# Kernel optimization log

Measured on AMD Instinct MI355X. Metric: run time of the kernel, lower is better.

Reference implementation:

```python
import jax, jax.numpy as jnp
import numpy as np

B, T, N, D = 32, 12, 325, 64
H = 4           # geo_num_heads == t_num_heads
HD = D // H     # head_dim = 16
M_SP = 32       # spatial frequency modes (min(32, N//2))
M_T = T // 2    # temporal frequency modes (all low modes)
SCALE = HD ** -0.5


def _lin(x, W):
    # torch nn.Linear (no bias): y = x @ W.T, W: [out, in]
    return jnp.einsum('btnd,ed->btne', x, W)


def _spatial(x, Wq, Wk, Wv, weights_Q, sp_modes):
    # FEDformer-style frequency attention over the node axis N
    q, k, v = _lin(x, Wq), _lin(x, Wk), _lin(x, Wv)          # [B,T,N,D]
    prep = lambda y: y.reshape(B, T, N, H, HD).transpose(0, 1, 3, 4, 2)  # [B,T,H,HD,N]
    qn = prep(q) / jnp.linalg.norm(q)   # global Frobenius norm (torch.norm with no dim)
    kn = prep(k) / jnp.linalg.norm(k)
    vn = prep(v)
    # rfft over nodes, gather selected modes (scatter-into-zeros in torch == gather here
    # since target indices are 0..M-1)
    qf = jnp.fft.rfft(qn, axis=-1)[..., sp_modes]            # [B,T,H,HD,M] c64
    kf = jnp.fft.rfft(kn, axis=-1)[..., sp_modes]
    vf = jnp.fft.rfft(vn, axis=-1)[..., sp_modes]
    M = M_SP
    qg = qf.transpose(0, 1, 2, 4, 3)[:, :, :, :, None, :]    # [B,T,H,M,1,HD]
    wq = jnp.broadcast_to(weights_Q.astype(jnp.complex64), (B, T, H, M, M - 1, HD))
    q_cat = jnp.concatenate([qg, wq], axis=4)                # [B,T,H,M,M,HD]
    kg = kf.transpose(0, 1, 2, 4, 3)[:, :, :, None, :, :]    # [B,T,H,1,M,HD]
    att = kg * jnp.conj(q_cat) * SCALE                       # [B,T,H,M,M,HD] c64
    att = jax.nn.softmax(jnp.abs(att), axis=-2).astype(jnp.complex64)
    att = att.transpose(0, 1, 2, 3, 5, 4)                    # [B,T,H,M,HD,M]
    vg = vf[:, :, :, None, :, :]                             # [B,T,H,1,HD,M]
    out = (vg * jnp.conj(att)).mean(axis=3)                  # [B,T,H,HD,M]
    out_ft = jnp.zeros((B, T, H, HD, N // 2 + 1), jnp.complex64).at[..., sp_modes].set(out)
    y = jnp.fft.irfft(out_ft, n=N, axis=-1)                  # [B,T,H,HD,N]
    return y.transpose(0, 1, 4, 2, 3).reshape(B, T, N, D)


def _temporal(x, Wq, Wk, Wv, weights_Q_t, t_modes):
    # frequency attention over the time axis T with causal (tril) mask.
    # NOTE: torch reshapes the [B,T,N,D] buffer directly as [B,N,T,H,HD] (raw view),
    # so we replicate that exact buffer reinterpretation.
    q, k, v = _lin(x, Wq), _lin(x, Wk), _lin(x, Wv)
    prep = lambda y: y.reshape(B, N, T, H, HD).transpose(0, 1, 3, 4, 2)  # [B,N,H,HD,T]
    qn = prep(q); kn = prep(k); vn = prep(v)
    qn = qn / jnp.linalg.norm(qn)
    kn = kn / jnp.linalg.norm(kn)
    qf = jnp.fft.rfft(qn, axis=-1)[..., t_modes]             # [B,N,H,HD,Mt]
    kf = jnp.fft.rfft(kn, axis=-1)[..., t_modes]
    vf = jnp.fft.rfft(vn, axis=-1)[..., t_modes]
    Mt = M_T
    qg = qf.transpose(0, 1, 2, 4, 3)[:, :, :, :, None, :]    # [B,N,H,Mt,1,HD]
    wq = jnp.broadcast_to(weights_Q_t.astype(jnp.complex64), (B, N, H, Mt, Mt - 1, HD))
    q_cat = jnp.concatenate([qg, wq], axis=4)                # [B,N,H,Mt,Mt,HD]
    kg = kf.transpose(0, 1, 2, 4, 3)[:, :, :, :, None, :]    # [B,N,H,Mt,1,HD] (unsqueeze(4) in torch)
    att = kg * jnp.conj(q_cat) * SCALE                       # [B,N,H,Mt,Mt,HD]
    att = att.transpose(0, 1, 2, 5, 3, 4)                    # [B,N,H,HD,Mt,Mt]
    mask = jnp.tril(jnp.ones((Mt, Mt), jnp.float32))
    att = att * mask                                         # zero above diagonal
    attw = jax.nn.softmax(jnp.abs(att), axis=-1).astype(jnp.complex64)
    vg = vf[..., None]                                       # [B,N,H,HD,Mt,1]
    out = (vg * jnp.conj(attw)).mean(axis=-1)                # [B,N,H,HD,Mt]
    out_ft = jnp.zeros((B, N, H, HD, T // 2 + 1), jnp.complex64).at[..., t_modes].set(out)
    y = jnp.fft.irfft(out_ft, n=T, axis=-1)                  # [B,N,H,HD,T]
    return y.transpose(0, 4, 1, 2, 3).reshape(B, T, N, D)


def _gcn(x, adj, W_fc1, W_mlp, b_mlp):
    a = adj / jnp.sum(adj, axis=1, keepdims=True)            # row-normalized
    agg = jnp.einsum('btkd,nk->btnd', x, a)
    h = jnp.einsum('btnd,ed->btne', agg, W_fc1)              # fc1 (no bias)
    return jnp.einsum('btnd,ed->btne', h, W_mlp) + b_mlp     # mlp (bias)


def _forward(x, adj, Wq_geo, Wk_geo, Wv_geo, Wq_t, Wk_t, Wv_t,
             W_fc1, W_mlp, b_mlp, weights_Q, weights_Q_t, sp_modes, t_modes):
    gcn_out = _gcn(x, adj, W_fc1, W_mlp, b_mlp)
    sp_x = _spatial(x, Wq_geo, Wk_geo, Wv_geo, weights_Q, sp_modes)
    te_x = _temporal(x, Wq_t, Wk_t, Wv_t, weights_Q_t, t_modes)
    return gcn_out + sp_x + te_x   # proj_drop is identity (p=0)


def setup_inputs() -> dict:
    key = jax.random.key(0)
    ks = jax.random.split(key, 13)
    w = lambda k, s: jax.random.normal(k, s, dtype=jnp.float32) * 0.05
    rng = np.random.default_rng(0)
    sp_modes = np.sort(rng.permutation(N // 2)[:M_SP]).astype(np.int32)
    t_modes = np.arange(M_T, dtype=np.int32)  # modes_T == T//2 selects all low modes
    return {
        'x': jax.random.normal(ks[0], (B, T, N, D), dtype=jnp.float32),
        'adj': jax.random.uniform(ks[1], (N, N), dtype=jnp.float32),
        'Wq_geo': w(ks[2], (D, D)), 'Wk_geo': w(ks[3], (D, D)), 'Wv_geo': w(ks[4], (D, D)),
        'Wq_t': w(ks[5], (D, D)), 'Wk_t': w(ks[6], (D, D)), 'Wv_t': w(ks[7], (D, D)),
        'W_fc1': w(ks[8], (D, D)), 'W_mlp': w(ks[9], (D, D)), 'b_mlp': w(ks[10], (D,)),
        'weights_Q': jax.random.normal(ks[11], (M_SP, M_SP - 1, HD), dtype=jnp.float32),
        'weights_Q_t': jax.random.normal(ks[12], (M_T, M_T - 1, HD), dtype=jnp.float32),
        'sp_modes': jnp.asarray(sp_modes),
        't_modes': jnp.asarray(t_modes),
    }


def reference(x, adj, Wq_geo, Wk_geo, Wv_geo, Wq_t, Wk_t, Wv_t,
              W_fc1, W_mlp, b_mlp, weights_Q, weights_Q_t, sp_modes, t_modes):
    return _forward(x, adj, Wq_geo, Wk_geo, Wv_geo, Wq_t, Wk_t, Wv_t,
                    W_fc1, W_mlp, b_mlp, weights_Q, weights_Q_t, sp_modes, t_modes)
```

## Files before the change

kernel.cpp:

```cpp
#include <hip/hip_runtime.h>


typedef unsigned short u16;
typedef short short8 __attribute__((ext_vector_type(8)));
typedef float floatx4 __attribute__((ext_vector_type(4)));

__device__ __forceinline__ u16 f2bf(float f) {
  union { float fp; unsigned int u; } v; v.fp = f;
  unsigned int x = v.u;
  x += 0x7FFF + ((x >> 16) & 1);
  return (u16)(x >> 16);
}

constexpr size_t OFF_NORM = 4096;
constexpr size_t OFF_WQA  = 8208;
constexpr size_t OFF_ANB  = 24080;
constexpr size_t OFF_TB   = 81280;
constexpr size_t OFF_T2   = 102080;
constexpr size_t OFF_OFT  = 112480;
constexpr size_t OFF_XCT  = 898912;
constexpr size_t OFF_WBB  = 5224288;
constexpr size_t OFF_WSPB = 5226336;
constexpr size_t OFF_WVTB = 5232480;
constexpr size_t OFF_XA   = 13211488;

__global__ __launch_bounds__(256) void k_prep(const float* __restrict__ x,
                                              const float* __restrict__ Wmlp,
                                              const float* __restrict__ Wfc1,
                                              const float* __restrict__ wQ,
                                              const float* __restrict__ Wq,
                                              const float* __restrict__ Wk,
                                              const float* __restrict__ Wv,
                                              const int* __restrict__ sp_modes,
                                              float* __restrict__ ws) {
  __shared__ float red[256];
  __shared__ __align__(16) u16 XA[128 * 72];
  const int tid = threadIdx.x;
  const int blk = blockIdx.x;
  u16* WBBu = (u16*)(ws + OFF_WBB);
  if (blk >= 22) {
    const int blk2 = blk - 22;
    const int wv = tid >> 6, lane = tid & 63, lc = lane & 15, quad = lane >> 4;
    const size_t base = (size_t)blk2 * 128;
    for (int i = tid; i < 2048; i += 256) {
      const int row = i >> 4, e0 = (i & 15) * 4;
      const float4 v = *(const float4*)(x + (base + row) * 64 + e0);
      u16* dst = &XA[row * 72 + e0];
      dst[0] = f2bf(v.x); dst[1] = f2bf(v.y); dst[2] = f2bf(v.z); dst[3] = f2bf(v.w);
    }
    __syncthreads();
    floatx4 acc[2][8] = {};
#pragma unroll
    for (int kc = 0; kc < 2; ++kc) {
      short8 af[2];
#pragma unroll
      for (int mi = 0; mi < 2; ++mi)
        af[mi] = *(const short8*)&XA[(32 * wv + 16 * mi + lc) * 72 + kc * 32 + quad * 8];
#pragma unroll
      for (int ni = 0; ni < 8; ++ni) {
        const int g = (ni & 3) * 16 + lc;
        const float* src = ((ni < 4) ? Wq : Wk) + (size_t)g * 64 + kc * 32 + quad * 8;
        float v8[8];
        *(float4*)v8 = *(const float4*)src;
        *(float4*)(v8 + 4) = *(const float4*)(src + 4);
        short8 bf_;
#pragma unroll
        for (int u = 0; u < 8; ++u) bf_[u] = (short)f2bf(v8[u]);
#pragma unroll
        for (int mi = 0; mi < 2; ++mi)
          acc[mi][ni] = __builtin_amdgcn_mfma_f32_16x16x32_bf16(af[mi], bf_, acc[mi][ni], 0, 0, 0);
      }
    }
    float sq = 0.f, sk = 0.f;
#pragma unroll
    for (int mi = 0; mi < 2; ++mi)
#pragma unroll
      for (int reg = 0; reg < 4; ++reg) {
#pragma unroll
        for (int ni = 0; ni < 4; ++ni) {
          const float v = acc[mi][ni][reg];
          sq = fmaf(v, v, sq);
        }
#pragma unroll
        for (int ni = 4; ni < 8; ++ni) {
          const float v = acc[mi][ni][reg];
          sk = fmaf(v, v, sk);
        }
      }
    for (int off = 32; off > 0; off >>= 1) {
      sq += __shfl_down(sq, off);
      sk += __shfl_down(sk, off);
    }
    if (lane == 0) { red[wv] = sq; red[8 + wv] = sk; }
    __syncthreads();
    if (tid == 0) {
      atomicAdd(&ws[OFF_NORM + 0], red[0] + red[1] + red[2] + red[3]);
      atomicAdd(&ws[OFF_NORM + 1], red[8] + red[9] + red[10] + red[11]);
    }
    return;
  }
  if (blk == 0) {
    for (int o = tid; o < 4096; o += 256) {
      int g = o >> 6, dd = o & 63;
      float s = 0.f;
      for (int e = 0; e < 64; ++e)
        s = fmaf(Wmlp[g * 64 + e], Wfc1[e * 64 + dd], s);
      WBBu[o] = f2bf(s);
    }
  } else if (blk < 9) {
    for (int i = (blk - 1) * 256 + tid; i < 15872; i += 2048)
      ws[OFF_WQA + i] = fabsf(wQ[i]);
  } else if (blk < 21) {
    const int j = blk - 9;
    u16* T2B = (u16*)(ws + OFF_T2);
    u16* TB = (u16*)(ws + OFF_TB);
    for (int jj = j; jj < 32; jj += 12) {
      const int f = sp_modes[jj];
      const float wgt = (f == 0) ? 1.f : 2.f;
      const int row_re = 8 * (jj >> 2) + (jj & 3);
      const int row_im = row_re + 4;
      for (int n = tid; n < 352; n += 256) {
        float c = 0.f, s = 0.f;
        if (n < 325) {
          int mm = (f * n) % 325;
          float th = 6.283185307179586f * (float)mm * (1.f / 325.f);
          c = cosf(th);
          s = sinf(th);
        }
        TB[(size_t)row_re * 352 + n] = f2bf(c);
        TB[(size_t)row_im * 352 + n] = f2bf(-s);
        if (n < 325) {
          T2B[(size_t)n * 64 + 2 * jj] = f2bf(wgt * (1.f / 325.f) * c);
          T2B[(size_t)n * 64 + 2 * jj + 1] = f2bf(-wgt * (1.f / 325.f) * s);
        }
      }
    }
  } else {
    u16* WSPBu = (u16*)(ws + OFF_WSPB);
    for (int i = tid; i < 12288; i += 256) {
      const int r = i >> 6, e = i & 63;
      const float* src = (r < 64) ? Wq : (r < 128) ? Wk : Wv;
      WSPBu[i] = f2bf(src[(size_t)(r & 63) * 64 + e]);
    }
  }
}

__global__ __launch_bounds__(256) void k_mega(const float* __restrict__ x,
                                              const float* __restrict__ adj,
                                              const float* __restrict__ Wvt,
                                              float* __restrict__ ws) {
  __shared__ __align__(16) float smem[12800];
  const int tid = threadIdx.x;
  const int blk = blockIdx.x;
  const int lane = tid & 63, wv = tid >> 6;
  const int lc = lane & 15, quad = lane >> 4;

  if (blk < 384) {
    const int bt = blk;
    u16* XBu = (u16*)smem;
    const float g_nq = ws[OFF_NORM + 0];
    const float g_nk = ws[OFF_NORM + 1];

    const u16* TB = (const u16*)(ws + OFF_TB);
    const u16* WSPBu = (const u16*)(ws + OFF_WSPB);
    const float* xb = x + (size_t)bt * 20800;
    const int br = tid & 31, be0 = (tid >> 5) * 8;

    {
      float va[4][8];
#pragma unroll
      for (int g = 0; g < 3; ++g) {
        const int nkc = (g < 2) ? 4 : 3;
#pragma unroll
        for (int u = 0; u < 4; ++u) {
          if (u >= nkc) break;
          const int k0 = (g * 4 + u) * 32;
          if (k0 + br < 325) {
            const float* src = xb + (size_t)(k0 + br) * 64 + be0;
            *(float4*)&va[u][0] = *(const float4*)src;
            *(float4*)&va[u][4] = *(const float4*)(src + 4);
          } else {
#pragma unroll
            for (int w = 0; w < 8; ++w) va[u][w] = 0.f;
          }
        }
#pragma unroll
        for (int u = 0; u < 4; ++u) {
          if (u >= nkc) break;
          const int k0 = (g * 4 + u) * 32;
#pragma unroll
          for (int w = 0; w < 8; ++w)
            XBu[(be0 + w) * 360 + k0 + br] = f2bf(va[u][w]);
        }
      }
    }
    __syncthreads();

    floatx4 accA[4] = {};
#pragma unroll
    for (int kc = 0; kc < 11; ++kc) {
      const short8 af = *(const short8*)&TB[(size_t)(16 * wv + lc) * 352 + kc * 32 + quad * 8];
#pragma unroll
      for (int t = 0; t < 4; ++t) {
        const short8 bf_ = *(const short8*)&XBu[(t * 16 + lc) * 360 + kc * 32 + quad * 8];
        accA[t] = __builtin_amdgcn_mfma_f32_16x16x32_bf16(af, bf_, accA[t], 0, 0, 0);
      }
    }
    __syncthreads();

    u16* xfl2 = XBu;
#pragma unroll
    for (int t = 0; t < 4; ++t)
#pragma unroll
      for (int r = 0; r < 4; ++r)
        xfl2[(t >> 1) * 2560 + (16 * wv + quad * 4 + r) * 40 + (t & 1) * 16 + lc] =
            f2bf(accA[t][r]);
    __syncthreads();

    floatx4 acc2[12] = {};
#pragma unroll
    for (int kc2 = 0; kc2 < 2; ++kc2) {
      const short8 af2 = *(const short8*)&xfl2[kc2 * 2560 + (16 * wv + lc) * 40 + quad * 8];
#pragma unroll
      for (int t = 0; t < 12; ++t) {
        const short8 bf2 = *(const short8*)&WSPBu[(t * 16 + lc) * 64 + kc2 * 32 + quad * 8];
        acc2[t] = __builtin_amdgcn_mfma_f32_16x16x32_bf16(af2, bf2, acc2[t], 0, 0, 0);
      }
    }
    __syncthreads();

    float* sq_q = smem + 2560;
    float* sq_k = smem + 4608;
    float* vfre = smem + 6656;
    float* vfim = smem + 8704;
    float* wbar = smem + 10752;
    for (int i = tid; i < 2048; i += 256) wbar[i] = 0.f;
    {
      const int fb = 8 * wv + ((quad >= 2) ? 4 : 0);
      const int isim = quad & 1;
#pragma unroll
      for (int t = 0; t < 12; ++t) {
        const int mat = t >> 2;
        const int d = (t & 3) * 16 + lc;
#pragma unroll
        for (int r = 0; r < 4; ++r) {
          const float v = acc2[t][r];
          if (mat == 2) {
            if (isim) vfim[(fb + r) * 64 + d] = v;
            else vfre[(fb + r) * 64 + d] = v;
          } else {
            const float s2 = v * v + __shfl_xor(v * v, 16);
            if (!isim) {
              if (mat == 0) sq_q[(fb + r) * 64 + d] = s2;
              else sq_k[(fb + r) * 64 + d] = s2;
            }
          }
        }
      }
    }
    __syncthreads();
    const float inv_nq = rsqrtf(g_nq);
    const float inv_nk = rsqrtf(g_nk);
    for (int i = tid; i < 2048; i += 256)
      sq_k[i] = 0.25f * inv_nk * sqrtf(sq_k[i]);
    __syncthreads();
    {
      const int d = tid & 63, fb2 = tid >> 6, hd = d & 15;
      const float* wqa = ws + OFF_WQA;
      float wacc[32];
#pragma unroll
      for (int j = 0; j < 32; ++j) wacc[j] = 0.f;
      for (int r8 = 0; r8 < 8; ++r8) {
        const int m = fb2 + (r8 << 2);
        const float aq = inv_nq * sqrtf(sq_q[m * 64 + d]);
        float sv[32];
        float mx = -1e30f;
#pragma unroll
        for (int j = 0; j < 32; ++j) {
          const float a = (j == 0) ? aq : wqa[(m * 31 + (j - 1)) * 16 + hd];
          const float s = sq_k[j * 64 + d] * a;
          sv[j] = s;
          mx = fmaxf(mx, s);
        }
        float sum = 0.f;
#pragma unroll
        for (int j = 0; j < 32; ++j) {
          const float ev = __expf(sv[j] - mx);
          sv[j] = ev;
          sum += ev;
        }
        const float sc = 0.03125f / sum;
#pragma unroll
        for (int j = 0; j < 32; ++j) wacc[j] += sv[j] * sc;
      }
#pragma unroll
      for (int j = 0; j < 32; ++j) atomicAdd(&wbar[j * 64 + d], wacc[j]);
    }
    __syncthreads();
    unsigned int* OFTu = (unsigned int*)(ws + OFF_OFT) + (size_t)bt * 2048;
    for (int i2 = tid; i2 < 2048; i2 += 256) {
      const int d = i2 >> 5, j = i2 & 31;
      const float w = wbar[j * 64 + d];
      const unsigned int lo = f2bf(vfre[j * 64 + d] * w);
      const unsigned int hi = f2bf(vfim[j * 64 + d] * w);
      OFTu[i2] = lo | (hi << 16);
    }
  } else if (blk < 1359) {
    const int blk2 = blk - 384;
    u16* XAu = (u16*)smem;
    const size_t base = (size_t)blk2 * 128;
    const u16* WBBu = (const u16*)(ws + OFF_WBB);

    for (int i = tid; i < 2048; i += 256) {
      const int row = i >> 4, e0 = (i & 15) * 4;
      const float4 v = *(const float4*)(x + (base + row) * 64 + e0);
      u16* dst = &XAu[row * 72 + e0];
      dst[0] = f2bf(v.x); dst[1] = f2bf(v.y); dst[2] = f2bf(v.z); dst[3] = f2bf(v.w);
    }
    __syncthreads();

    floatx4 acc[2][4] = {};
#pragma unroll
    for (int kc = 0; kc < 2; ++kc) {
      short8 af[2];
#pragma unroll
      for (int mi = 0; mi < 2; ++mi)
        af[mi] = *(const short8*)&XAu[(32 * wv + 16 * mi + lc) * 72 + kc * 32 + quad * 8];
#pragma unroll
      for (int ni = 0; ni < 4; ++ni) {
        const short8 bf_ = *(const short8*)&WBBu[(ni * 16 + lc) * 64 + kc * 32 + quad * 8];
#pragma unroll
        for (int mi = 0; mi < 2; ++mi)
          acc[mi][ni] = __builtin_amdgcn_mfma_f32_16x16x32_bf16(af[mi], bf_, acc[mi][ni], 0, 0, 0);
      }
    }
    __syncthreads();

    u16* xcT = XAu;
#pragma unroll
    for (int ni = 0; ni < 4; ++ni)
#pragma unroll
      for (int mi = 0; mi < 2; ++mi)
#pragma unroll
        for (int reg = 0; reg < 4; ++reg)
          xcT[(ni * 16 + lc) * 132 + 32 * wv + 16 * mi + quad * 4 + reg] =
              f2bf(acc[mi][ni][reg]);
    __syncthreads();
    u16* XCT = (u16*)(ws + OFF_XCT);
    for (int i = tid; i < 8192; i += 256) {
      const int d = i >> 7, r = i & 127;
      const unsigned int row = (unsigned int)(base + r);
      const unsigned int bt = row / 325u;
      const unsigned int n = row - bt * 325u;
      XCT[(size_t)bt * 22528 + (size_t)d * 352 + n] = xcT[d * 132 + r];
    }
  } else if (blk < 2009) {
    const int idx = (blk - 1359) * 256 + tid;
    if (idx >= 32 * 325 * 16) return;
    const int dq = idx & 15;
    const int n = (idx >> 4) % 325;
    const int b = idx / (16 * 325);
    const float* xp = x + ((size_t)b * 3900 + (size_t)n * 12) * 64 + dq * 4;
    float4 s = make_float4(0.f, 0.f, 0.f, 0.f);
    float sign = 1.f;
    for (int k = 0; k < 12; ++k) {
      const float4 v = *(const float4*)(xp + (size_t)k * 64);
      s.x += sign * v.x; s.y += sign * v.y; s.z += sign * v.z; s.w += sign * v.w;
      sign = -sign;
    }
    *(float4*)(ws + OFF_XA + ((size_t)b * 325 + n) * 64 + dq * 4) = s;
  } else if (blk < 2334) {
    const int n = blk - 2009;
    float* red = smem;
    float p = 0.f;
    for (int k = tid; k < 325; k += 256) p += adj[n * 325 + k];
    red[tid] = p;
    __syncthreads();
    for (int s2 = 128; s2 > 0; s2 >>= 1) {
      if (tid < s2) red[tid] += red[tid + s2];
      __syncthreads();
    }
    const float inv = 1.f / red[0];
    u16* ANB = (u16*)(ws + OFF_ANB);
    for (int k = tid; k < 352; k += 256)
      ANB[(size_t)n * 352 + k] = (k < 325) ? f2bf(adj[n * 325 + k] * inv) : (u16)0;
  } else if (blk < 2430) {
    const int idx = (blk - 2334) * 256 + tid;
    u16* p = (u16*)(ws + OFF_XCT) + (size_t)(idx >> 6) * 22528 + (size_t)(idx & 63) * 352;
    for (int c = 325; c < 352; ++c) p[c] = 0;
  } else {
    u16* WVTBu = (u16*)(ws + OFF_WVTB);
    for (int i = tid; i < 4096; i += 256) WVTBu[i] = f2bf(Wvt[i]);
  }
}

__global__ __launch_bounds__(256) void k_final2(const float* __restrict__ x,
                                                const float* __restrict__ bmlp,
                                                float* __restrict__ ws,
                                                float* __restrict__ out) {
  const int tid = threadIdx.x;
  const int bt = blockIdx.x / 3, mc = blockIdx.x % 3;
  const int m0 = mc * 128;
  const int wave = tid >> 6, lane = tid & 63;
  const int quad = lane >> 4, lc = lane & 15;

  const u16* ANB = (const u16*)(ws + OFF_ANB);
  const u16* T2B = (const u16*)(ws + OFF_T2);
  const u16* XCT = (const u16*)(ws + OFF_XCT) + (size_t)bt * 22528;
  const u16* OFT = (const u16*)(ws + OFF_OFT) + (size_t)bt * 4096;
  const u16* WVTBu = (const u16*)(ws + OFF_WVTB);

  const int b = bt / 12, t = bt - b * 12;
  const float sgn12 = ((t & 1) ? -1.f : 1.f) * (1.f / 12.f);

  floatx4 acc[2][4] = {};

#pragma unroll
  for (int c13 = 0; c13 < 13; ++c13) {
    const bool gcn = (c13 < 11);
    const u16* Asrc = gcn ? ANB : T2B;
    const int astr = gcn ? 352 : 64;
    const int acol = gcn ? c13 * 32 : (c13 - 11) * 32;
    const u16* Bsrc = gcn ? XCT : OFT;
    const int bstr = gcn ? 352 : 64;
    short8 af[2], bf_[4];
#pragma unroll
    for (int mi = 0; mi < 2; ++mi) {
      const int gr = m0 + wave * 32 + mi * 16 + lc;
      short8 a = {};
      if (gr < 325)
        a = *(const short8*)&Asrc[(size_t)gr * astr + acol + quad * 8];
      af[mi] = a;
    }
#pragma unroll
    for (int ni = 0; ni < 4; ++ni)
      bf_[ni] = *(const short8*)&Bsrc[(size_t)(ni * 16 + lc) * bstr + acol + quad * 8];
#pragma unroll
    for (int mi = 0; mi < 2; ++mi)
#pragma unroll
      for (int ni = 0; ni < 4; ++ni)
        acc[mi][ni] = __builtin_amdgcn_mfma_f32_16x16x32_bf16(
            af[mi], bf_[ni], acc[mi][ni], 0, 0, 0);
  }

#pragma unroll
  for (int kc = 0; kc < 2; ++kc) {
    const int k0 = kc * 32 + quad * 8;
    short8 af[2];
#pragma unroll
    for (int mi = 0; mi < 2; ++mi) {
      const int nr = m0 + wave * 32 + mi * 16 + lc;
      short8 a = {};
      if (nr < 325) {
        const float* xp = x + ((size_t)b * 3900 + (size_t)nr * 12 + t) * 64 + k0;
        const float* xap = ws + OFF_XA + ((size_t)b * 325 + nr) * 64 + k0;
        float xv[8], av[8];
        *(float4*)xv = *(const float4*)xp;
        *(float4*)(xv + 4) = *(const float4*)(xp + 4);
        *(float4*)av = *(const float4*)xap;
        *(float4*)(av + 4) = *(const float4*)(xap + 4);
#pragma unroll
        for (int u = 0; u < 8; ++u)
          a[u] = (short)f2bf((xv[u] - sgn12 * av[u]) * (1.f / 6.f));
      }
      af[mi] = a;
    }
#pragma unroll
    for (int ni = 0; ni < 4; ++ni) {
      const short8 bf_ = *(const short8*)&WVTBu[(size_t)(ni * 16 + lc) * 64 + k0];
#pragma unroll
      for (int mi = 0; mi < 2; ++mi)
        acc[mi][ni] = __builtin_amdgcn_mfma_f32_16x16x32_bf16(
            af[mi], bf_, acc[mi][ni], 0, 0, 0);
    }
  }

#pragma unroll
  for (int ni = 0; ni < 4; ++ni) {
    const int d = ni * 16 + lc;
    const float bias = bmlp[d];
#pragma unroll
    for (int mi = 0; mi < 2; ++mi) {
#pragma unroll
      for (int reg = 0; reg < 4; ++reg) {
        const int n = m0 + wave * 32 + mi * 16 + quad * 4 + reg;
        if (n >= 325) continue;
        out[((size_t)bt * 325 + n) * 64 + d] = acc[mi][ni][reg] + bias;
      }
    }
  }
}

extern "C" void kernel_launch(void* const* d_in, const int* in_sizes, int n_in,
                              void* d_out, int out_size, void* d_ws, size_t ws_size,
                              hipStream_t stream) {
  const float* x = (const float*)d_in[0];
  const float* adj = (const float*)d_in[1];
  const float* Wq_g = (const float*)d_in[2];
  const float* Wk_g = (const float*)d_in[3];
  const float* Wv_g = (const float*)d_in[4];
  const float* Wv_t = (const float*)d_in[7];
  const float* Wfc1 = (const float*)d_in[8];
  const float* Wmlp = (const float*)d_in[9];
  const float* bmlp = (const float*)d_in[10];
  const float* wQ = (const float*)d_in[11];
  const int* sp_modes = (const int*)d_in[13];
  float* ws = (float*)d_ws;
  float* out = (float*)d_out;

  (void)in_sizes; (void)n_in; (void)out_size; (void)ws_size;

  hipMemsetAsync(ws + OFF_NORM, 0, 2 * sizeof(float), stream);
  k_prep<<<997, 256, 0, stream>>>(x, Wmlp, Wfc1, wQ, Wq_g, Wk_g, Wv_g,
                                  sp_modes, ws);
  k_mega<<<2431, 256, 0, stream>>>(x, adj, Wv_t, ws);
  k_final2<<<1152, 256, 0, stream>>>(x, bmlp, ws, out);
}
```

Measured before the change: 250.9 us.

## Fuse norm reduction into mega kernel and move spectral softmax into final kernel

```diff
diff --git a/kernel.cpp b/kernel.cpp
--- a/kernel.cpp
+++ b/kernel.cpp
@@ -17,15 +17,17 @@
 constexpr size_t OFF_ANB  = 24080;
 constexpr size_t OFF_TB   = 81280;
 constexpr size_t OFF_T2   = 102080;
-constexpr size_t OFF_OFT  = 112480;
 constexpr size_t OFF_XCT  = 898912;
 constexpr size_t OFF_WBB  = 5224288;
-constexpr size_t OFF_WSPB = 5226336;
-constexpr size_t OFF_WVTB = 5232480;
+constexpr size_t OFF_WSPB = 5230432;
+constexpr size_t OFF_WVTB = 5236576;
+constexpr size_t OFF_SQQ  = 5240000;
+constexpr size_t OFF_SQK  = 6026432;
+constexpr size_t OFF_VFR  = 6812864;
+constexpr size_t OFF_VFI  = 7599296;
 constexpr size_t OFF_XA   = 13211488;
 
-__global__ __launch_bounds__(256) void k_prep(const float* __restrict__ x,
-                                              const float* __restrict__ Wmlp,
+__global__ __launch_bounds__(256) void k_prep(const float* __restrict__ Wmlp,
                                               const float* __restrict__ Wfc1,
                                               const float* __restrict__ wQ,
                                               const float* __restrict__ Wq,
@@ -33,73 +35,11 @@
                                               const float* __restrict__ Wv,
                                               const int* __restrict__ sp_modes,
                                               float* __restrict__ ws) {
-  __shared__ float red[256];
-  __shared__ __align__(16) u16 XA[128 * 72];
   const int tid = threadIdx.x;
   const int blk = blockIdx.x;
   u16* WBBu = (u16*)(ws + OFF_WBB);
-  if (blk >= 22) {
-    const int blk2 = blk - 22;
-    const int wv = tid >> 6, lane = tid & 63, lc = lane & 15, quad = lane >> 4;
-    const size_t base = (size_t)blk2 * 128;
-    for (int i = tid; i < 2048; i += 256) {
-      const int row = i >> 4, e0 = (i & 15) * 4;
-      const float4 v = *(const float4*)(x + (base + row) * 64 + e0);
-      u16* dst = &XA[row * 72 + e0];
-      dst[0] = f2bf(v.x); dst[1] = f2bf(v.y); dst[2] = f2bf(v.z); dst[3] = f2bf(v.w);
-    }
-    __syncthreads();
-    floatx4 acc[2][8] = {};
-#pragma unroll
-    for (int kc = 0; kc < 2; ++kc) {
-      short8 af[2];
-#pragma unroll
-      for (int mi = 0; mi < 2; ++mi)
-        af[mi] = *(const short8*)&XA[(32 * wv + 16 * mi + lc) * 72 + kc * 32 + quad * 8];
-#pragma unroll
-      for (int ni = 0; ni < 8; ++ni) {
-        const int g = (ni & 3) * 16 + lc;
-        const float* src = ((ni < 4) ? Wq : Wk) + (size_t)g * 64 + kc * 32 + quad * 8;
-        float v8[8];
-        *(float4*)v8 = *(const float4*)src;
-        *(float4*)(v8 + 4) = *(const float4*)(src + 4);
-        short8 bf_;
-#pragma unroll
-        for (int u = 0; u < 8; ++u) bf_[u] = (short)f2bf(v8[u]);
-#pragma unroll
-        for (int mi = 0; mi < 2; ++mi)
-          acc[mi][ni] = __builtin_amdgcn_mfma_f32_16x16x32_bf16(af[mi], bf_, acc[mi][ni], 0, 0, 0);
-      }
-    }
-    float sq = 0.f, sk = 0.f;
-#pragma unroll
-    for (int mi = 0; mi < 2; ++mi)
-#pragma unroll
-      for (int reg = 0; reg < 4; ++reg) {
-#pragma unroll
-        for (int ni = 0; ni < 4; ++ni) {
-          const float v = acc[mi][ni][reg];
-          sq = fmaf(v, v, sq);
-        }
-#pragma unroll
-        for (int ni = 4; ni < 8; ++ni) {
-          const float v = acc[mi][ni][reg];
-          sk = fmaf(v, v, sk);
-        }
-      }
-    for (int off = 32; off > 0; off >>= 1) {
-      sq += __shfl_down(sq, off);
-      sk += __shfl_down(sk, off);
-    }
-    if (lane == 0) { red[wv] = sq; red[8 + wv] = sk; }
-    __syncthreads();
-    if (tid == 0) {
-      atomicAdd(&ws[OFF_NORM + 0], red[0] + red[1] + red[2] + red[3]);
-      atomicAdd(&ws[OFF_NORM + 1], red[8] + red[9] + red[10] + red[11]);
-    }
-    return;
-  }
   if (blk == 0) {
+    for (int i = tid; i < 512; i += 256) ws[OFF_NORM + i] = 0.f;
     for (int o = tid; o < 4096; o += 256) {
       int g = o >> 6, dd = o & 63;
       float s = 0.f;
@@ -135,13 +75,19 @@
         }
       }
     }
-  } else {
+  } else if (blk == 21) {
     u16* WSPBu = (u16*)(ws + OFF_WSPB);
     for (int i = tid; i < 12288; i += 256) {
       const int r = i >> 6, e = i & 63;
       const float* src = (r < 64) ? Wq : (r < 128) ? Wk : Wv;
       WSPBu[i] = f2bf(src[(size_t)(r & 63) * 64 + e]);
     }
+  } else {
+    for (int i = tid; i < 8192; i += 256) {
+      const int r = i >> 6, e = i & 63;
+      const float* src = (r < 64) ? Wq : Wk;
+      WBBu[4096 + i] = f2bf(src[(size_t)(r & 63) * 64 + e]);
+    }
   }
 }
 
@@ -149,7 +95,7 @@
                                               const float* __restrict__ adj,
                                               const float* __restrict__ Wvt,
                                               float* __restrict__ ws) {
-  __shared__ __align__(16) float smem[12800];
+  __shared__ __align__(16) float smem[11520];
   const int tid = threadIdx.x;
   const int blk = blockIdx.x;
   const int lane = tid & 63, wv = tid >> 6;
@@ -158,8 +104,6 @@
   if (blk < 384) {
     const int bt = blk;
     u16* XBu = (u16*)smem;
-    const float g_nq = ws[OFF_NORM + 0];
-    const float g_nk = ws[OFF_NORM + 1];
 
     const u16* TB = (const u16*)(ws + OFF_TB);
     const u16* WSPBu = (const u16*)(ws + OFF_WSPB);
@@ -227,14 +171,11 @@
         acc2[t] = __builtin_amdgcn_mfma_f32_16x16x32_bf16(af2, bf2, acc2[t], 0, 0, 0);
       }
     }
-    __syncthreads();
-
-    float* sq_q = smem + 2560;
-    float* sq_k = smem + 4608;
-    float* vfre = smem + 6656;
-    float* vfim = smem + 8704;
-    float* wbar = smem + 10752;
-    for (int i = tid; i < 2048; i += 256) wbar[i] = 0.f;
+
+    float* g_sqq = ws + OFF_SQQ + (size_t)bt * 2048;
+    float* g_sqk = ws + OFF_SQK + (size_t)bt * 2048;
+    float* g_vfr = ws + OFF_VFR + (size_t)bt * 2048;
+    float* g_vfi = ws + OFF_VFI + (size_t)bt * 2048;
     {
       const int fb = 8 * wv + ((quad >= 2) ? 4 : 0);
       const int isim = quad & 1;
@@ -246,68 +187,22 @@
         for (int r = 0; r < 4; ++r) {
           const float v = acc2[t][r];
           if (mat == 2) {
-            if (isim) vfim[(fb + r) * 64 + d] = v;
-            else vfre[(fb + r) * 64 + d] = v;
+            if (isim) g_vfi[(fb + r) * 64 + d] = v;
+            else g_vfr[(fb + r) * 64 + d] = v;
           } else {
             const float s2 = v * v + __shfl_xor(v * v, 16);
             if (!isim) {
-              if (mat == 0) sq_q[(fb + r) * 64 + d] = s2;
-              else sq_k[(fb + r) * 64 + d] = s2;
+              if (mat == 0) g_sqq[(fb + r) * 64 + d] = sqrtf(s2);
+              else g_sqk[(fb + r) * 64 + d] = sqrtf(s2);
             }
           }
         }
       }
     }
-    __syncthreads();
-    const float inv_nq = rsqrtf(g_nq);
-    const float inv_nk = rsqrtf(g_nk);
-    for (int i = tid; i < 2048; i += 256)
-      sq_k[i] = 0.25f * inv_nk * sqrtf(sq_k[i]);
-    __syncthreads();
-    {
-      const int d = tid & 63, fb2 = tid >> 6, hd = d & 15;
-      const float* wqa = ws + OFF_WQA;
-      float wacc[32];
-#pragma unroll
-      for (int j = 0; j < 32; ++j) wacc[j] = 0.f;
-      for (int r8 = 0; r8 < 8; ++r8) {
-        const int m = fb2 + (r8 << 2);
-        const float aq = inv_nq * sqrtf(sq_q[m * 64 + d]);
-        float sv[32];
-        float mx = -1e30f;
-#pragma unroll
-        for (int j = 0; j < 32; ++j) {
-          const float a = (j == 0) ? aq : wqa[(m * 31 + (j - 1)) * 16 + hd];
-          const float s = sq_k[j * 64 + d] * a;
-          sv[j] = s;
-          mx = fmaxf(mx, s);
-        }
-        float sum = 0.f;
-#pragma unroll
-        for (int j = 0; j < 32; ++j) {
-          const float ev = __expf(sv[j] - mx);
-          sv[j] = ev;
-          sum += ev;
-        }
-        const float sc = 0.03125f / sum;
-#pragma unroll
-        for (int j = 0; j < 32; ++j) wacc[j] += sv[j] * sc;
-      }
-#pragma unroll
-      for (int j = 0; j < 32; ++j) atomicAdd(&wbar[j * 64 + d], wacc[j]);
-    }
-    __syncthreads();
-    unsigned int* OFTu = (unsigned int*)(ws + OFF_OFT) + (size_t)bt * 2048;
-    for (int i2 = tid; i2 < 2048; i2 += 256) {
-      const int d = i2 >> 5, j = i2 & 31;
-      const float w = wbar[j * 64 + d];
-      const unsigned int lo = f2bf(vfre[j * 64 + d] * w);
-      const unsigned int hi = f2bf(vfim[j * 64 + d] * w);
-      OFTu[i2] = lo | (hi << 16);
-    }
   } else if (blk < 1359) {
     const int blk2 = blk - 384;
     u16* XAu = (u16*)smem;
+    float* red = smem + 4608;
     const size_t base = (size_t)blk2 * 128;
     const u16* WBBu = (const u16*)(ws + OFF_WBB);
 
@@ -319,21 +214,46 @@
     }
     __syncthreads();
 
+    short8 afc[2][2];
+#pragma unroll
+    for (int kc = 0; kc < 2; ++kc)
+#pragma unroll
+      for (int mi = 0; mi < 2; ++mi)
+        afc[mi][kc] = *(const short8*)&XAu[(32 * wv + 16 * mi + lc) * 72 + kc * 32 + quad * 8];
+
     floatx4 acc[2][4] = {};
 #pragma unroll
-    for (int kc = 0; kc < 2; ++kc) {
-      short8 af[2];
-#pragma unroll
-      for (int mi = 0; mi < 2; ++mi)
-        af[mi] = *(const short8*)&XAu[(32 * wv + 16 * mi + lc) * 72 + kc * 32 + quad * 8];
+    for (int kc = 0; kc < 2; ++kc)
 #pragma unroll
       for (int ni = 0; ni < 4; ++ni) {
         const short8 bf_ = *(const short8*)&WBBu[(ni * 16 + lc) * 64 + kc * 32 + quad * 8];
 #pragma unroll
         for (int mi = 0; mi < 2; ++mi)
-          acc[mi][ni] = __builtin_amdgcn_mfma_f32_16x16x32_bf16(af[mi], bf_, acc[mi][ni], 0, 0, 0);
-      }
-    }
+          acc[mi][ni] = __builtin_amdgcn_mfma_f32_16x16x32_bf16(afc[mi][kc], bf_, acc[mi][ni], 0, 0, 0);
+      }
+
+    float sq = 0.f, sk = 0.f;
+#pragma unroll
+    for (int ni = 0; ni < 8; ++ni) {
+      floatx4 a0 = {}, a1 = {};
+#pragma unroll
+      for (int kc = 0; kc < 2; ++kc) {
+        const short8 bf_ = *(const short8*)&WBBu[
+            (size_t)(64 + (ni >> 2) * 64 + (ni & 3) * 16 + lc) * 64 + kc * 32 + quad * 8];
+        a0 = __builtin_amdgcn_mfma_f32_16x16x32_bf16(afc[0][kc], bf_, a0, 0, 0, 0);
+        a1 = __builtin_amdgcn_mfma_f32_16x16x32_bf16(afc[1][kc], bf_, a1, 0, 0, 0);
+      }
+      float s = 0.f;
+#pragma unroll
+      for (int reg = 0; reg < 4; ++reg)
+        s = fmaf(a0[reg], a0[reg], fmaf(a1[reg], a1[reg], s));
+      if (ni < 4) sq += s; else sk += s;
+    }
+    for (int off = 32; off > 0; off >>= 1) {
+      sq += __shfl_down(sq, off);
+      sk += __shfl_down(sk, off);
+    }
+    if (lane == 0) { red[wv] = sq; red[8 + wv] = sk; }
     __syncthreads();
 
     u16* xcT = XAu;
@@ -354,6 +274,12 @@
       const unsigned int n = row - bt * 325u;
       XCT[(size_t)bt * 22528 + (size_t)d * 352 + n] = xcT[d * 132 + r];
     }
+    if (tid == 0)
+      atomicAdd(&ws[OFF_NORM + 32 * (size_t)(blk2 & 15) + 0],
+                red[0] + red[1] + red[2] + red[3]);
+    if (tid == 1)
+      atomicAdd(&ws[OFF_NORM + 32 * (size_t)(blk2 & 15) + 1],
+                red[8] + red[9] + red[10] + red[11]);
   } else if (blk < 2009) {
     const int idx = (blk - 1359) * 256 + tid;
     if (idx >= 32 * 325 * 16) return;
@@ -394,20 +320,83 @@
   }
 }
 
-__global__ __launch_bounds__(256) void k_final2(const float* __restrict__ x,
+__global__ __launch_bounds__(256) void k_final3(const float* __restrict__ x,
                                                 const float* __restrict__ bmlp,
                                                 float* __restrict__ ws,
                                                 float* __restrict__ out) {
+  __shared__ __align__(16) float smem[8448];
+  float* asq = smem;
+  float* askl = smem + 2048;
+  float* wbar = smem + 4096;
+  unsigned int* oftu = (unsigned int*)(smem + 6144);
+  const u16* oft16 = (const u16*)oftu;
+
   const int tid = threadIdx.x;
   const int bt = blockIdx.x / 3, mc = blockIdx.x % 3;
   const int m0 = mc * 128;
   const int wave = tid >> 6, lane = tid & 63;
   const int quad = lane >> 4, lc = lane & 15;
 
+  float nq = 0.f, nk = 0.f;
+#pragma unroll
+  for (int k2 = 0; k2 < 16; ++k2) {
+    const float2 v = *(const float2*)(ws + OFF_NORM + 32 * (size_t)k2);
+    nq += v.x; nk += v.y;
+  }
+  const float inv_nq = rsqrtf(nq);
+  const float inv_nk = rsqrtf(nk);
+
+  for (int i = tid; i < 2048; i += 256) {
+    asq[i] = ws[OFF_SQQ + (size_t)bt * 2048 + i];
+    askl[i] = 0.25f * inv_nk * ws[OFF_SQK + (size_t)bt * 2048 + i];
+    wbar[i] = 0.f;
+  }
+  __syncthreads();
+  {
+    const int d = tid & 63, fb2 = tid >> 6, hd = d & 15;
+    const float* wqa = ws + OFF_WQA;
+    float wacc[32];
+#pragma unroll
+    for (int j = 0; j < 32; ++j) wacc[j] = 0.f;
+    for (int r8 = 0; r8 < 8; ++r8) {
+      const int m = fb2 + (r8 << 2);
+      const float aq = inv_nq * asq[m * 64 + d];
+      float sv[32];
+      float mx = -1e30f;
+#pragma unroll
+      for (int j = 0; j < 32; ++j) {
+        const float a = (j == 0) ? aq : wqa[(m * 31 + (j - 1)) * 16 + hd];
+        const float s = askl[j * 64 + d] * a;
+        sv[j] = s;
+        mx = fmaxf(mx, s);
+      }
+      float sum = 0.f;
+#pragma unroll
+      for (int j = 0; j < 32; ++j) {
+        const float ev = __expf(sv[j] - mx);
+        sv[j] = ev;
+        sum += ev;
+      }
+      const float sc = 0.03125f / sum;
+#pragma unroll
+      for (int j = 0; j < 32; ++j) wacc[j] += sv[j] * sc;
+    }
+#pragma unroll
+    for (int j = 0; j < 32; ++j) atomicAdd(&wbar[j * 64 + d], wacc[j]);
+  }
+  __syncthreads();
+  for (int i2 = tid; i2 < 2048; i2 += 256) {
+    const int j = i2 >> 6, d = i2 & 63;
+    const float w = wbar[j * 64 + d];
+    const unsigned int lo = f2bf(ws[OFF_VFR + (size_t)bt * 2048 + j * 64 + d] * w);
+    const unsigned int hi = f2bf(ws[OFF_VFI + (size_t)bt * 2048 + j * 64 + d] * w);
+    oftu[d * 36 + j] = lo | (hi << 16);
+  }
+  __syncthreads();
+
   const u16* ANB = (const u16*)(ws + OFF_ANB);
   const u16* T2B = (const u16*)(ws + OFF_T2);
   const u16* XCT = (const u16*)(ws + OFF_XCT) + (size_t)bt * 22528;
-  const u16* OFT = (const u16*)(ws + OFF_OFT) + (size_t)bt * 4096;
   const u16* WVTBu = (const u16*)(ws + OFF_WVTB);
 
   const int b = bt / 12, t = bt - b * 12;
@@ -418,23 +407,21 @@
 #pragma unroll
   for (int c13 = 0; c13 < 13; ++c13) {
     const bool gcn = (c13 < 11);
-    const u16* Asrc = gcn ? ANB : T2B;
-    const int astr = gcn ? 352 : 64;
     const int acol = gcn ? c13 * 32 : (c13 - 11) * 32;
-    const u16* Bsrc = gcn ? XCT : OFT;
-    const int bstr = gcn ? 352 : 64;
     short8 af[2], bf_[4];
 #pragma unroll
     for (int mi = 0; mi < 2; ++mi) {
       const int gr = m0 + wave * 32 + mi * 16 + lc;
       short8 a = {};
       if (gr < 325)
-        a = *(const short8*)&Asrc[(size_t)gr * astr + acol + quad * 8];
+        a = gcn ? *(const short8*)&ANB[(size_t)gr * 352 + acol + quad * 8]
+                : *(const short8*)&T2B[(size_t)gr * 64 + acol + quad * 8];
       af[mi] = a;
     }
 #pragma unroll
     for (int ni = 0; ni < 4; ++ni)
-      bf_[ni] = *(const short8*)&Bsrc[(size_t)(ni * 16 + lc) * bstr + acol + quad * 8];
+      bf_[ni] = gcn ? *(const short8*)&XCT[(size_t)(ni * 16 + lc) * 352 + acol + quad * 8]
+                    : *(const short8*)&oft16[(ni * 16 + lc) * 72 + acol + quad * 8];
 #pragma unroll
     for (int mi = 0; mi < 2; ++mi)
 #pragma unroll
@@ -510,9 +497,7 @@
 
   (void)in_sizes; (void)n_in; (void)out_size; (void)ws_size;
 
-  hipMemsetAsync(ws + OFF_NORM, 0, 2 * sizeof(float), stream);
-  k_prep<<<997, 256, 0, stream>>>(x, Wmlp, Wfc1, wQ, Wq_g, Wk_g, Wv_g,
-                                  sp_modes, ws);
+  k_prep<<<23, 256, 0, stream>>>(Wmlp, Wfc1, wQ, Wq_g, Wk_g, Wv_g, sp_modes, ws);
   k_mega<<<2431, 256, 0, stream>>>(x, adj, Wv_t, ws);
-  k_final2<<<1152, 256, 0, stream>>>(x, bmlp, ws, out);
+  k_final3<<<1152, 256, 0, stream>>>(x, bmlp, ws, out);
 }
```

New measurement: 281.1 us. 12.0% more time.
